# Kernel tuning notes

Hardware: AMD Instinct MI355X
Metric: run time of the kernel (lower is better)

Reference implementation:

```python
import jax, jax.numpy as jnp
import numpy as np

B, T, P, D, H, L, C = 32, 50000, 100, 512, 16, 6, 256
SCALES = [1, 2, 4]
NS = len(SCALES)
HS = H // NS          # heads per scale = 5
KD = D // H           # key_dim = 32
N = T // P            # num_patches = 500
FF = 4 * D
EPS = 1e-3            # keras LayerNormalization default epsilon


def layernorm(x, g, b):
    m = jnp.mean(x, axis=-1, keepdims=True)
    v = jnp.var(x, axis=-1, keepdims=True)
    return (x - m) * jax.lax.rsqrt(v + EPS) * g + b


def mha(x, Wq, bq, Wk, bk, Wv, bv, Wo, bo):
    # keras MultiHeadAttention: self-attention, scale 1/sqrt(key_dim), biases on
    q = jnp.einsum('bnd,dhk->bnhk', x, Wq) + bq
    k = jnp.einsum('bnd,dhk->bnhk', x, Wk) + bk
    v = jnp.einsum('bnd,dhk->bnhk', x, Wv) + bv
    scores = jnp.einsum('bnhk,bmhk->bhnm', q, k) / jnp.sqrt(jnp.asarray(KD, x.dtype))
    p = jax.nn.softmax(scores, axis=-1)
    o = jnp.einsum('bhnm,bmhk->bnhk', p, v)
    return jnp.einsum('bnhk,hkd->bnd', o, Wo) + bo


def forward(inputs, ln_in_g, ln_in_b, patch_W, patch_b, pos_emb,
            Wq, bq, Wk, bk, Wv, bv, Wo, bo, Wc, bc,
            ln1_g, ln1_b, W1, b1, W2, b2, ln2_g, ln2_b, head_W, head_b):
    x = inputs[..., None]                       # (B, T, 1)
    x = layernorm(x, ln_in_g, ln_in_b)          # degenerate size-1 LN (faithful)
    patches = x.reshape(B, N, P)                # (B, N, P)
    h = patches @ patch_W + patch_b + pos_emb   # (B, N, D)
    for l in range(L):
        outs = []
        for si, s in enumerate(SCALES):
            if s > 1:
                pooled = h.reshape(B, N // s, s, D).mean(axis=2)  # SAME avg_pool1d (N % s == 0)
            else:
                pooled = h
            a = mha(pooled, Wq[l, si], bq[l, si], Wk[l, si], bk[l, si],
                    Wv[l, si], bv[l, si], Wo[l, si], bo[l, si])
            if s > 1:
                a = jnp.repeat(a, s, axis=1)[:, :N]
            outs.append(a)
        comb = jnp.concatenate(outs, axis=-1) @ Wc[l] + bc[l]
        h = h + comb
        h = layernorm(h, ln1_g[l], ln1_b[l])
        f = jax.nn.gelu(h @ W1[l] + b1[l], approximate=False)
        f = f @ W2[l] + b2[l]
        h = h + f
        h = layernorm(h, ln2_g[l], ln2_b[l])
        # Dropout(0.1) identity at inference
    g = h.mean(axis=1)                          # GlobalAveragePooling1D
    return jax.nn.softmax(g @ head_W + head_b, axis=-1)  # key head


def setup_inputs() -> dict:
    key = jax.random.key(0)
    ks = jax.random.split(key, 20)
    r = lambda k, sh, s=0.02: (jax.random.normal(k, sh, jnp.float32) * s)
    f32 = jnp.float32
    return {
        'inputs': jax.random.normal(ks[0], (B, T), f32),
        'ln_in_g': jnp.ones((1,), f32),
        'ln_in_b': r(ks[1], (1,)),
        'patch_W': r(ks[2], (P, D)),
        'patch_b': r(ks[3], (D,)),
        'pos_emb': r(ks[4], (1, N, D)),
        'Wq': r(ks[5], (L, NS, D, HS, KD)), 'bq': jnp.zeros((L, NS, HS, KD), f32),
        'Wk': r(ks[6], (L, NS, D, HS, KD)), 'bk': jnp.zeros((L, NS, HS, KD), f32),
        'Wv': r(ks[7], (L, NS, D, HS, KD)), 'bv': jnp.zeros((L, NS, HS, KD), f32),
        'Wo': r(ks[8], (L, NS, HS, KD, D)), 'bo': jnp.zeros((L, NS, D), f32),
        'Wc': r(ks[9], (L, NS * D, D)), 'bc': jnp.zeros((L, D), f32),
        'ln1_g': jnp.ones((L, D), f32), 'ln1_b': jnp.zeros((L, D), f32),
        'W1': r(ks[10], (L, D, FF)), 'b1': jnp.zeros((L, FF), f32),
        'W2': r(ks[11], (L, FF, D)), 'b2': jnp.zeros((L, D), f32),
        'ln2_g': jnp.ones((L, D), f32), 'ln2_b': jnp.zeros((L, D), f32),
        'head_W': r(ks[12], (D, C)), 'head_b': jnp.zeros((C,), f32),
    }


def reference(inputs, ln_in_g, ln_in_b, patch_W, patch_b, pos_emb,
              Wq, bq, Wk, bk, Wv, bv, Wo, bo, Wc, bc,
              ln1_g, ln1_b, W1, b1, W2, b2, ln2_g, ln2_b, head_W, head_b):
    return forward(inputs, ln_in_g, ln_in_b, patch_W, patch_b, pos_emb,
                   Wq, bq, Wk, bk, Wv, bv, Wo, bo, Wc, bc,
                   ln1_g, ln1_b, W1, b1, W2, b2, ln2_g, ln2_b, head_W, head_b)
```

## Files before the change

### kernel.cpp

```cpp
#include <hip/hip_runtime.h>
#include <math.h>


#define DD 512
#define NN 500
#define HSC 5
#define KDD 32
#define QKVN 160
#define QKV3 480
#define FF 2048
#define NL 6
#define NC 256
#define NB 32
#define LNEPS 1e-3f
#define BM 128
#define BN 64
#define KCHB 64

#define AOFF1 256000
#define AOFF2 384000
#define RTOT 875
#define OSZ 140000
#define MLSZ 4384
#define QSP 420000

typedef __attribute__((ext_vector_type(8))) short bf16x8;
typedef __attribute__((ext_vector_type(4))) float f32x4;

__device__ __forceinline__ float gelu_exact(float x) {
    return 0.5f * x * (1.0f + erff(x * 0.70710678118654752f));
}

__device__ __forceinline__ unsigned int pkbf(float a, float b) {
    unsigned int r;
    asm("v_cvt_pk_bf16_f32 %0, %1, %2" : "=v"(r) : "v"(a), "v"(b));
    return r;
}


template<int POOL, int GATHER, int TAIL>
__device__ __forceinline__ void mstage(
        const float* __restrict__ A, int lda,
        const float* __restrict__ Bcol, int ldb,
        int M, int bm, int k0, int klim,
        int ar4, int akq, int bkq,
        float4 (&aR)[2][4], float4 (&bR)[4]) {
    #pragma unroll
    for (int p = 0; p < 2; ++p) {
        int row = min(bm + ar4 + p * 64, M - 1);
        const float* ap;
        if (!GATHER) {
            ap = A + (size_t)row * POOL * lda;
        } else {
            int si = k0 >> 9;
            ap = A + (si == 0 ? 0 : (si == 1 ? AOFF1 : AOFF2))
               + (size_t)(row >> si) * DD - (size_t)(k0 & ~(DD - 1));
        }
        #pragma unroll
        for (int i = 0; i < 4; ++i) {
            int kk = akq + i * 4;
            int kg = TAIL ? min(k0 + kk, klim - 4) : (k0 + kk);
            float4 v = *(const float4*)(ap + kg);
            #pragma unroll
            for (int t = 1; t < POOL; ++t) {
                float4 u = *(const float4*)(ap + kg + (size_t)t * lda);
                v.x += u.x; v.y += u.y; v.z += u.z; v.w += u.w;
            }
            if (POOL > 1) {
                const float ip = 1.0f / (float)POOL;
                v.x *= ip; v.y *= ip; v.z *= ip; v.w *= ip;
            }
            if (TAIL) {
                bool ok = (k0 + kk) < klim;
                v.x = ok ? v.x : 0.f; v.y = ok ? v.y : 0.f;
                v.z = ok ? v.z : 0.f; v.w = ok ? v.w : 0.f;
            }
            aR[p][i] = v;
        }
    }
    #pragma unroll
    for (int i = 0; i < 4; ++i) {
        int kr = TAIL ? min(k0 + bkq + i, klim - 1) : (k0 + bkq + i);
        bR[i] = *(const float4*)(Bcol + (size_t)kr * ldb);
    }
}

template<int POOL, int GATHER, int TAIL>
__device__ __forceinline__ void mfma_core(
        const float* __restrict__ A, int lda,
        const float* __restrict__ Bcol, int ldb,
        int M, int bm, int ks, int nch, int klim, f32x4 (&acc)[4][2]) {
    __shared__ __align__(16) unsigned short As[128 * 64];
    __shared__ __align__(16) unsigned short Bs[64 * 64];
    const int tid = threadIdx.x;
    const int ar4 = tid >> 2, akq = (tid & 3) * 16;
    const int bkq = (tid >> 4) * 4, bn4 = tid & 15;
    const int lane = tid & 63, wid = tid >> 6;
    const int wm = wid >> 1, wn = wid & 1;

    float4 aR[2][4], bR[4];
    mstage<POOL, GATHER, TAIL>(A, lda, Bcol, ldb, M, bm, ks, klim,
                               ar4, akq, bkq, aR, bR);

    for (int c = 0; c < nch; ++c) {
        __syncthreads();
        #pragma unroll
        for (int p = 0; p < 2; ++p) {
            int r = ar4 + p * 64;
            int swz = (r & 7) << 4;
            char* base = (char*)As + r * 128;
            #pragma unroll
            for (int i = 0; i < 4; ++i) {
                int cb = (akq + i * 4) * 2;
                *(uint2*)(base + (cb ^ swz)) = make_uint2(
                    pkbf(aR[p][i].x, aR[p][i].y), pkbf(aR[p][i].z, aR[p][i].w));
            }
        }
        {
            const float* b0 = (const float*)&bR[0];
            const float* b1 = (const float*)&bR[1];
            const float* b2 = (const float*)&bR[2];
            const float* b3 = (const float*)&bR[3];
            #pragma unroll
            for (int j = 0; j < 4; ++j) {
                int nrow = bn4 * 4 + j;
                char* base = (char*)Bs + nrow * 128;
                *(uint2*)(base + ((bkq * 2) ^ ((nrow & 7) << 4))) = make_uint2(
                    pkbf(b0[j], b1[j]), pkbf(b2[j], b3[j]));
            }
        }
        __syncthreads();
        if (c + 1 < nch)
            mstage<POOL, GATHER, TAIL>(A, lda, Bcol, ldb, M, bm,
                                       ks + (c + 1) * KCHB, klim,
                                       ar4, akq, bkq, aR, bR);
        #pragma unroll
        for (int half = 0; half < 2; ++half) {
            const int kb = (half * 32 + (lane >> 4) * 8) * 2;
            bf16x8 af[4], bf[2];
            #pragma unroll
            for (int m = 0; m < 4; ++m) {
                int r = wm * 64 + m * 16 + (lane & 15);
                af[m] = *(const bf16x8*)((const char*)As + r * 128 + (kb ^ ((r & 7) << 4)));
            }
            #pragma unroll
            for (int n = 0; n < 2; ++n) {
                int r = wn * 32 + n * 16 + (lane & 15);
                bf[n] = *(const bf16x8*)((const char*)Bs + r * 128 + (kb ^ ((r & 7) << 4)));
            }
            #pragma unroll
            for (int m = 0; m < 4; ++m)
                #pragma unroll
                for (int n = 0; n < 2; ++n)
                    acc[m][n] = __builtin_amdgcn_mfma_f32_16x16x32_bf16(
                        af[m], bf[n], acc[m][n], 0, 0, 0);
        }
    }
}

#define MACC_INIT(acc) { _Pragma("unroll") for (int m_ = 0; m_ < 4; ++m_) \
    _Pragma("unroll") for (int n_ = 0; n_ < 2; ++n_) \
    _Pragma("unroll") for (int j_ = 0; j_ < 4; ++j_) acc[m_][n_][j_] = 0.f; }

__global__ void colsum_kernel(const float* __restrict__ pw, float* __restrict__ csum) {
    int d = blockIdx.x * blockDim.x + threadIdx.x;
    if (d < DD) {
        float s = 0.f;
        for (int p = 0; p < 100; ++p) s += pw[p * DD + d];
        csum[d] = s;
    }
}

__global__ void init_h(const float* __restrict__ csum, const float* __restrict__ pb,
                       const float* __restrict__ pos, const float* __restrict__ lnb,
                       float* __restrict__ h) {
    int idx = blockIdx.x * 256 + threadIdx.x;
    if (idx >= NN * DD) return;
    int d = idx & (DD - 1);
    h[idx] = lnb[0] * csum[d] + pb[d] + pos[idx];
}

__global__ __launch_bounds__(256, 2) void qkv_part(
        const float* __restrict__ h,
        const float* __restrict__ Wq, const float* __restrict__ Wk,
        const float* __restrict__ Wv,
        float* __restrict__ part, int l) {
    int scale = blockIdx.z >> 2, ps = blockIdx.z & 3;
    int n = NN >> scale;
    int bm = blockIdx.y * BM;
    if (bm >= n) return;
    int bn = blockIdx.x * BN;
    size_t w = (size_t)(l * 3 + scale);
    int tid = threadIdx.x;
    int col = min(bn + (tid & 15) * 4, QKV3 - 4);
    int which = (col >= 320) ? 2 : ((col >= 160) ? 1 : 0);
    const float* Wsel = (which == 0) ? Wq : ((which == 1) ? Wk : Wv);
    const float* Bcol = Wsel + w * DD * QKVN + (col - which * QKVN);
    float* outb = part + (size_t)ps * QSP
                + (scale == 0 ? 0 : (scale == 1 ? 240000 : 360000));

    f32x4 acc[4][2];
    MACC_INIT(acc);
    if (scale == 0)
        mfma_core<1, 0, 0>(h, DD, Bcol, QKVN, n, bm, ps * 128, 2, DD, acc);
    else if (scale == 1)
        mfma_core<2, 0, 0>(h, DD, Bcol, QKVN, n, bm, ps * 128, 2, DD, acc);
    else
        mfma_core<4, 0, 0>(h, DD, Bcol, QKVN, n, bm, ps * 128, 2, DD, acc);

    int lane = tid & 63, wid = tid >> 6, wm = wid >> 1, wn = wid & 1;
    #pragma unroll
    for (int q = 0; q < 2; ++q) {
        int cb = bn + wn * 32 + q * 16;
        if (cb >= QKV3) continue;
        int c2 = cb + (lane & 15);
        #pragma unroll
        for (int m = 0; m < 4; ++m) {
            int r0 = bm + wm * 64 + m * 16 + ((lane >> 4) << 2);
            #pragma unroll
            for (int j = 0; j < 4; ++j) {
                int r = r0 + j;
                if (r < n) outb[(size_t)r * QKV3 + c2] = acc[m][q][j];
            }
        }
    }
}

__global__ void qkv_reduce(const float* __restrict__ part,
                           const float* __restrict__ bq,
                           const float* __restrict__ bk,
                           const float* __restrict__ bv,
                           float* __restrict__ qkvAll, int l) {
    int idx = blockIdx.x * 256 + threadIdx.x;
    if (idx >= 420000) return;
    int scale, base;
    if (idx < 240000) { scale = 0; base = 0; }
    else if (idx < 360000) { scale = 1; base = 240000; }
    else { scale = 2; base = 360000; }
    int rowrem = (idx - base) % QKV3;
    int which = rowrem / QKVN;
    int col = rowrem - which * QKVN;
    float v = part[idx] + part[QSP + idx]
            + part[2 * QSP + idx] + part[3 * QSP + idx];
    v += ((which == 0) ? bq : (which == 1 ? bk : bv))[(size_t)(l * 3 + scale) * QKVN + col];
    qkvAll[idx] = v;
}

__global__ __launch_bounds__(256, 2) void attn_split(
        const float* __restrict__ qkvAll, float* __restrict__ oPart,
        float* __restrict__ mPart, float* __restrict__ lPart) {
    int z = blockIdx.z;
    int scale, sp;
    if (z < 8)       { scale = 0; sp = z; }
    else if (z < 12) { scale = 1; sp = z - 8; }
    else             { scale = 2; sp = z - 12; }
    int n = NN >> scale;
    int qt = blockIdx.x;
    if (qt * 64 >= n) return;
    int hh = blockIdx.y;
    int ks = sp * 64;
    int ke = min(n, ks + 64);
    const float* qkv = qkvAll + (scale == 0 ? 0 : (scale == 1 ? 240000 : 360000));
    int rowb = (scale == 0 ? 0 : (scale == 1 ? 500 : 750));

    int tid = threadIdx.x;
    int kg = tid & 7, qq = tid >> 3;
    int q0 = qt * 64 + qq, q1 = q0 + 32;
    bool ok0 = q0 < n, ok1 = q1 < n;

    float qa[32], qb[32];
    {
        const float* p0 = qkv + (size_t)(ok0 ? q0 : 0) * QKV3 + hh * KDD;
        const float* p1 = qkv + (size_t)(ok1 ? q1 : 0) * QKV3 + hh * KDD;
        #pragma unroll
        for (int c4 = 0; c4 < 8; ++c4) {
            float4 v0 = *(const float4*)(p0 + c4 * 4);
            float4 v1 = *(const float4*)(p1 + c4 * 4);
            qa[c4 * 4] = v0.x; qa[c4 * 4 + 1] = v0.y; qa[c4 * 4 + 2] = v0.z; qa[c4 * 4 + 3] = v0.w;
            qb[c4 * 4] = v1.x; qb[c4 * 4 + 1] = v1.y; qb[c4 * 4 + 2] = v1.z; qb[c4 * 4 + 3] = v1.w;
        }
    }

    __shared__ float Ks[64][36];
    __shared__ float Vs[64][36];
    float o0[32], o1[32];
    #pragma unroll
    for (int c = 0; c < 32; ++c) { o0[c] = 0.f; o1[c] = 0.f; }
    float m0 = -1e30f, m1 = -1e30f, l0 = 0.f, l1 = 0.f;

    int srow = tid >> 2, scol = tid & 3;

    {
        int kc = ks;
        int krow = kc + srow;
        bool ok = krow < ke;
        const float* kp = qkv + (size_t)(ok ? krow : 0) * QKV3 + QKVN + hh * KDD;
        #pragma unroll
        for (int half = 0; half < 2; ++half) {
            int cc = (half * 4 + scol) * 4;
            float4 kv = ok ? *(const float4*)(kp + cc) : make_float4(0.f, 0.f, 0.f, 0.f);
            float4 vv = ok ? *(const float4*)(kp + QKVN + cc) : make_float4(0.f, 0.f, 0.f, 0.f);
            Ks[srow][cc] = kv.x; Ks[srow][cc + 1] = kv.y; Ks[srow][cc + 2] = kv.z; Ks[srow][cc + 3] = kv.w;
            Vs[srow][cc] = vv.x; Vs[srow][cc + 1] = vv.y; Vs[srow][cc + 2] = vv.z; Vs[srow][cc + 3] = vv.w;
        }
        __syncthreads();

        float p0[8], p1[8];
        float cm = -1e30f;
        #pragma unroll
        for (int jj = 0; jj < 8; ++jj) {
            int j = jj * 8 + kg;
            float s0 = 0.f, s1 = 0.f;
            #pragma unroll
            for (int c4 = 0; c4 < 8; ++c4) {
                float4 kv = *(const float4*)&Ks[j][c4 * 4];
                s0 += qa[c4 * 4] * kv.x + qa[c4 * 4 + 1] * kv.y
                    + qa[c4 * 4 + 2] * kv.z + qa[c4 * 4 + 3] * kv.w;
                s1 += qb[c4 * 4] * kv.x + qb[c4 * 4 + 1] * kv.y
                    + qb[c4 * 4 + 2] * kv.z + qb[c4 * 4 + 3] * kv.w;
            }
            s0 *= 0.17677669529663687f;
            s1 *= 0.17677669529663687f;
            if (kc + j >= ke) { s0 = -1e30f; s1 = -1e30f; }
            p0[jj] = s0; p1[jj] = s1;
            cm = fmaxf(cm, fmaxf(s0, s1));
        }
        cm = fmaxf(cm, __shfl_xor(cm, 1));
        cm = fmaxf(cm, __shfl_xor(cm, 2));
        cm = fmaxf(cm, __shfl_xor(cm, 4));

        m0 = cm; m1 = cm;
        #pragma unroll
        for (int jj = 0; jj < 8; ++jj) {
            p0[jj] = expf(p0[jj] - cm); l0 += p0[jj];
            p1[jj] = expf(p1[jj] - cm); l1 += p1[jj];
        }
        #pragma unroll
        for (int jj = 0; jj < 8; ++jj) {
            int j = jj * 8 + kg;
            float w0 = p0[jj], w1 = p1[jj];
            #pragma unroll
            for (int c4 = 0; c4 < 8; ++c4) {
                float4 vv = *(const float4*)&Vs[j][c4 * 4];
                o0[c4 * 4]     += w0 * vv.x; o0[c4 * 4 + 1] += w0 * vv.y;
                o0[c4 * 4 + 2] += w0 * vv.z; o0[c4 * 4 + 3] += w0 * vv.w;
                o1[c4 * 4]     += w1 * vv.x; o1[c4 * 4 + 1] += w1 * vv.y;
                o1[c4 * 4 + 2] += w1 * vv.z; o1[c4 * 4 + 3] += w1 * vv.w;
            }
        }
    }
    #pragma unroll
    for (int st = 1; st < 8; st <<= 1) {
        l0 += __shfl_xor(l0, st);
        l1 += __shfl_xor(l1, st);
        #pragma unroll
        for (int c = 0; c < 32; ++c) {
            o0[c] += __shfl_xor(o0[c], st);
            o1[c] += __shfl_xor(o1[c], st);
        }
    }
    if (kg == 0) {
        float* ob = oPart + (size_t)sp * OSZ;
        if (ok0) {
            int r = rowb + q0;
            float* op = ob + (size_t)r * QKVN + hh * KDD;
            #pragma unroll
            for (int c4 = 0; c4 < 8; ++c4) {
                float4 v; v.x = o0[c4*4]; v.y = o0[c4*4+1]; v.z = o0[c4*4+2]; v.w = o0[c4*4+3];
                *(float4*)(op + c4 * 4) = v;
            }
            mPart[sp * MLSZ + r * HSC + hh] = m0;
            lPart[sp * MLSZ + r * HSC + hh] = l0;
        }
        if (ok1) {
            int r = rowb + q1;
            float* op = ob + (size_t)r * QKVN + hh * KDD;
            #pragma unroll
            for (int c4 = 0; c4 < 8; ++c4) {
                float4 v; v.x = o1[c4*4]; v.y = o1[c4*4+1]; v.z = o1[c4*4+2]; v.w = o1[c4*4+3];
                *(float4*)(op + c4 * 4) = v;
            }
            mPart[sp * MLSZ + r * HSC + hh] = m1;
            lPart[sp * MLSZ + r * HSC + hh] = l1;
        }
    }
}

__global__ void attn_combine(const float* __restrict__ oPart,
                             const float* __restrict__ mPart,
                             const float* __restrict__ lPart,
                             float* __restrict__ oAll) {
    int idx = blockIdx.x * 256 + threadIdx.x;
    if (idx >= OSZ) return;
    int rh = idx >> 5;
    int r = rh / HSC, hh = rh - r * HSC;
    int scale = (r < 500) ? 0 : (r < 750 ? 1 : 2);
    int ns = 8 >> scale;
    float M = -1e30f;
    for (int s = 0; s < ns; ++s) M = fmaxf(M, mPart[s * MLSZ + r * HSC + hh]);
    float L = 0.f, val = 0.f;
    for (int s = 0; s < ns; ++s) {
        float wgt = expf(mPart[s * MLSZ + r * HSC + hh] - M);
        L += wgt * lPart[s * MLSZ + r * HSC + hh];
        val += wgt * oPart[(size_t)s * OSZ + idx];
    }
    oAll[idx] = val / L;
}

__global__ __launch_bounds__(256, 2) void wo_all(
        const float* __restrict__ oAll, const float* __restrict__ Wo,
        const float* __restrict__ bo, float* __restrict__ aAll, int l) {
    int z = blockIdx.z;
    int n = NN >> z;
    int bm = blockIdx.y * BM;
    if (bm >= n) return;
    int bn = blockIdx.x * BN;
    size_t w = (size_t)(l * 3 + z);
    const float* A = oAll + (z == 0 ? 0 : (z == 1 ? 80000 : 120000));
    float* C = aAll + (z == 0 ? 0 : (z == 1 ? AOFF1 : AOFF2));
    int tid = threadIdx.x;
    const float* Bcol = Wo + w * QKVN * DD + bn + (tid & 15) * 4;

    f32x4 acc[4][2];
    MACC_INIT(acc);
    mfma_core<1, 0, 32>(A, QKVN, Bcol, DD, n, bm, 0, 3, QKVN, acc);

    const float* bias = bo + w * DD;
    int lane = tid & 63, wid = tid >> 6, wm = wid >> 1, wn = wid & 1;
    #pragma unroll
    for (int q = 0; q < 2; ++q) {
        int c2 = bn + wn * 32 + q * 16 + (lane & 15);
        float bv_ = bias[c2];
        #pragma unroll
        for (int m = 0; m < 4; ++m) {
            int r0 = bm + wm * 64 + m * 16 + ((lane >> 4) << 2);
            #pragma unroll
            for (int j = 0; j < 4; ++j) {
                int r = r0 + j;
                if (r < n) C[(size_t)r * DD + c2] = acc[m][q][j] + bv_;
            }
        }
    }
}

__global__ __launch_bounds__(256, 2) void comb_part(
        const float* __restrict__ aAll, const float* __restrict__ Wc,
        float* __restrict__ part) {
    int zz = blockIdx.z;
    int bm = blockIdx.y * BM, bn = blockIdx.x * BN;
    int tid = threadIdx.x;
    const float* Bcol = Wc + bn + (tid & 15) * 4;
    f32x4 acc[4][2];
    MACC_INIT(acc);
    mfma_core<1, 1, 0>(aAll, DD, Bcol, DD, NN, bm, zz * 128, 2, 1536, acc);

    float* pz = part + (size_t)zz * NN * DD;
    int lane = tid & 63, wid = tid >> 6, wm = wid >> 1, wn = wid & 1;
    #pragma unroll
    for (int q = 0; q < 2; ++q) {
        int c2 = bn + wn * 32 + q * 16 + (lane & 15);
        #pragma unroll
        for (int m = 0; m < 4; ++m) {
            int r0 = bm + wm * 64 + m * 16 + ((lane >> 4) << 2);
            #pragma unroll
            for (int j = 0; j < 4; ++j) {
                int r = r0 + j;
                if (r < NN) pz[(size_t)r * DD + c2] = acc[m][q][j];
            }
        }
    }
}

__global__ __launch_bounds__(256, 2) void w1_part(
        const float* __restrict__ h, const float* __restrict__ W1,
        float* __restrict__ part) {
    int sp = blockIdx.z;
    int bm = blockIdx.y * BM, bn = blockIdx.x * BN;
    int tid = threadIdx.x;
    const float* Bcol = W1 + bn + (tid & 15) * 4;
    f32x4 acc[4][2];
    MACC_INIT(acc);
    mfma_core<1, 0, 0>(h, DD, Bcol, FF, NN, bm, sp * 128, 2, DD, acc);

    float* pz = part + (size_t)sp * NN * FF;
    int lane = tid & 63, wid = tid >> 6, wm = wid >> 1, wn = wid & 1;
    #pragma unroll
    for (int q = 0; q < 2; ++q) {
        int c2 = bn + wn * 32 + q * 16 + (lane & 15);
        #pragma unroll
        for (int m = 0; m < 4; ++m) {
            int r0 = bm + wm * 64 + m * 16 + ((lane >> 4) << 2);
            #pragma unroll
            for (int j = 0; j < 4; ++j) {
                int r = r0 + j;
                if (r < NN) pz[(size_t)r * FF + c2] = acc[m][q][j];
            }
        }
    }
}

__global__ void w1_reduce(const float* __restrict__ part,
                          const float* __restrict__ b1, float* __restrict__ f) {
    int idx = blockIdx.x * 256 + threadIdx.x;
    if (idx >= NN * FF) return;
    float v = part[idx] + part[NN * FF + idx]
            + part[2 * NN * FF + idx] + part[3 * NN * FF + idx];
    f[idx] = gelu_exact(v + b1[idx & (FF - 1)]);
}

__global__ __launch_bounds__(256, 2) void w2_part(
        const float* __restrict__ f, const float* __restrict__ W2,
        float* __restrict__ part) {
    int sp = blockIdx.z;
    int bm = blockIdx.y * BM, bn = blockIdx.x * BN;
    int tid = threadIdx.x;
    const float* Bcol = W2 + bn + (tid & 15) * 4;
    f32x4 acc[4][2];
    MACC_INIT(acc);
    mfma_core<1, 0, 0>(f, FF, Bcol, DD, NN, bm, sp * 128, 2, FF, acc);

    float* pz = part + (size_t)sp * NN * DD;
    int lane = tid & 63, wid = tid >> 6, wm = wid >> 1, wn = wid & 1;
    #pragma unroll
    for (int q = 0; q < 2; ++q) {
        int c2 = bn + wn * 32 + q * 16 + (lane & 15);
        #pragma unroll
        for (int m = 0; m < 4; ++m) {
            int r0 = bm + wm * 64 + m * 16 + ((lane >> 4) << 2);
            #pragma unroll
            for (int j = 0; j < 4; ++j) {
                int r = r0 + j;
                if (r < NN) pz[(size_t)r * DD + c2] = acc[m][q][j];
            }
        }
    }
}

__global__ void reduce_add_ln(const float* __restrict__ part, int S,
                              const float* __restrict__ bias,
                              float* __restrict__ h,
                              const float* __restrict__ gw,
                              const float* __restrict__ bw) {
    int row = blockIdx.x, t = threadIdx.x;
    size_t idx = (size_t)row * DD + t;
    float x = h[idx] + bias[t];
    for (int s = 0; s < S; ++s) x += part[(size_t)s * NN * DD + idx];
    int lane = t & 63, wv = t >> 6;
    __shared__ float s1[8], s2[8];
    __shared__ float mb[2];
    float sum = x, sq = x * x;
    for (int off = 32; off; off >>= 1) {
        sum += __shfl_down(sum, off);
        sq  += __shfl_down(sq,  off);
    }
    if (lane == 0) { s1[wv] = sum; s2[wv] = sq; }
    __syncthreads();
    if (t == 0) {
        float a = 0.f, b = 0.f;
        for (int i = 0; i < 8; ++i) { a += s1[i]; b += s2[i]; }
        float mean = a / (float)DD;
        float var = b / (float)DD - mean * mean;
        mb[0] = mean;
        mb[1] = rsqrtf(var + LNEPS);
    }
    __syncthreads();
    h[idx] = (x - mb[0]) * mb[1] * gw[t] + bw[t];
}

__global__ void col_mean_part(const float* __restrict__ h, float* __restrict__ partial) {
    int col = blockIdx.x * 256 + threadIdx.x;
    int r0 = blockIdx.y * 20;
    float s = 0.f;
    #pragma unroll
    for (int r = 0; r < 20; ++r) s += h[(size_t)(r0 + r) * DD + col];
    partial[(size_t)blockIdx.y * DD + col] = s;
}

__global__ void head_kernel(const float* __restrict__ partial,
                            const float* __restrict__ hw,
                            const float* __restrict__ hb, float* __restrict__ out) {
    __shared__ float gs[DD];
    __shared__ float r[4];
    __shared__ float bmx, bsum;
    int t = threadIdx.x;
    for (int d = t; d < DD; d += 256) {
        float s = 0.f;
        #pragma unroll
        for (int p = 0; p < 25; ++p) s += partial[(size_t)p * DD + d];
        gs[d] = s / (float)NN;
    }
    __syncthreads();
    float acc = hb[t];
    #pragma unroll 16
    for (int d = 0; d < DD; ++d) acc += gs[d] * hw[(size_t)d * NC + t];
    int lane = t & 63, wv = t >> 6;
    float mx = acc;
    for (int off = 32; off; off >>= 1) mx = fmaxf(mx, __shfl_down(mx, off));
    if (lane == 0) r[wv] = mx;
    __syncthreads();
    if (t == 0) bmx = fmaxf(fmaxf(r[0], r[1]), fmaxf(r[2], r[3]));
    __syncthreads();
    float e = expf(acc - bmx);
    float s = e;
    for (int off = 32; off; off >>= 1) s += __shfl_down(s, off);
    if (lane == 0) r[wv] = s;
    __syncthreads();
    if (t == 0) bsum = 1.f / (r[0] + r[1] + r[2] + r[3]);
    __syncthreads();
    float pv = e * bsum;
    for (int b = 0; b < NB; ++b) out[(size_t)b * NC + t] = pv;
}

extern "C" void kernel_launch(void* const* d_in, const int* in_sizes, int n_in,
                              void* d_out, int out_size, void* d_ws, size_t ws_size,
                              hipStream_t stream) {
    const float* ln_in_b = (const float*)d_in[2];
    const float* patch_W = (const float*)d_in[3];
    const float* patch_b = (const float*)d_in[4];
    const float* pos_emb = (const float*)d_in[5];
    const float* Wq = (const float*)d_in[6];
    const float* bq = (const float*)d_in[7];
    const float* Wk = (const float*)d_in[8];
    const float* bk = (const float*)d_in[9];
    const float* Wv = (const float*)d_in[10];
    const float* bv = (const float*)d_in[11];
    const float* Wo = (const float*)d_in[12];
    const float* bo = (const float*)d_in[13];
    const float* Wc = (const float*)d_in[14];
    const float* bc = (const float*)d_in[15];
    const float* ln1_g = (const float*)d_in[16];
    const float* ln1_b = (const float*)d_in[17];
    const float* W1 = (const float*)d_in[18];
    const float* b1 = (const float*)d_in[19];
    const float* W2 = (const float*)d_in[20];
    const float* b2 = (const float*)d_in[21];
    const float* ln2_g = (const float*)d_in[22];
    const float* ln2_b = (const float*)d_in[23];
    const float* head_W = (const float*)d_in[24];
    const float* head_b = (const float*)d_in[25];
    float* out = (float*)d_out;

    float* ws = (float*)d_ws;
    float* h      = ws;
    float* csum   = h + 256000;
    float* qkvAll = csum + 1024;
    float* oAll   = qkvAll + 420000;
    float* aAll   = oAll + 140000;
    float* f      = aAll + 448000;
    float* part   = f + 1024000;
    float* headp  = part + 4194304;
    float* qkvP   = part;
    float* oPart  = part + 1680000;
    float* mPart  = oPart + 1120000;
    float* lPart  = mPart + 8 * MLSZ;

    colsum_kernel<<<1, 512, 0, stream>>>(patch_W, csum);
    init_h<<<(NN * DD + 255) / 256, 256, 0, stream>>>(csum, patch_b, pos_emb, ln_in_b, h);

    for (int l = 0; l < NL; ++l) {
        qkv_part<<<dim3(8, 4, 12), 256, 0, stream>>>(h, Wq, Wk, Wv, qkvP, l);
        qkv_reduce<<<(420000 + 255) / 256, 256, 0, stream>>>(qkvP, bq, bk, bv, qkvAll, l);
        attn_split<<<dim3(8, HSC, 14), 256, 0, stream>>>(qkvAll, oPart, mPart, lPart);
        attn_combine<<<(OSZ + 255) / 256, 256, 0, stream>>>(oPart, mPart, lPart, oAll);
        wo_all<<<dim3(8, 4, 3), 256, 0, stream>>>(oAll, Wo, bo, aAll, l);
        comb_part<<<dim3(8, 4, 12), 256, 0, stream>>>(
            aAll, Wc + (size_t)l * 3 * DD * DD, part);
        reduce_add_ln<<<NN, DD, 0, stream>>>(part, 12, bc + (size_t)l * DD, h,
                                             ln1_g + (size_t)l * DD, ln1_b + (size_t)l * DD);
        w1_part<<<dim3(32, 4, 4), 256, 0, stream>>>(
            h, W1 + (size_t)l * DD * FF, part);
        w1_reduce<<<(NN * FF + 255) / 256, 256, 0, stream>>>(
            part, b1 + (size_t)l * FF, f);
        w2_part<<<dim3(8, 4, 16), 256, 0, stream>>>(f, W2 + (size_t)l * FF * DD, part);
        reduce_add_ln<<<NN, DD, 0, stream>>>(part, 16, b2 + (size_t)l * DD, h,
                                             ln2_g + (size_t)l * DD, ln2_b + (size_t)l * DD);
    }
    col_mean_part<<<dim3(2, 25), 256, 0, stream>>>(h, headp);
    head_kernel<<<1, 256, 0, stream>>>(headp, head_W, head_b, out);
}
```

Baseline: 783.6 us.

## Fold Wo into Wc weights so attention outputs feed the combine GEMM directly

```diff
diff --git a/kernel.cpp b/kernel.cpp
--- a/kernel.cpp
+++ b/kernel.cpp
@@ -17,12 +17,11 @@
 #define BN 64
 #define KCHB 64
 
-#define AOFF1 256000
-#define AOFF2 384000
 #define RTOT 875
 #define OSZ 140000
 #define MLSZ 4384
 #define QSP 420000
+#define W2CL 98304
 
 typedef __attribute__((ext_vector_type(8))) short bf16x8;
 typedef __attribute__((ext_vector_type(4))) float f32x4;
@@ -38,7 +37,7 @@
 }
 
 
-template<int POOL, int GATHER, int TAIL>
+template<int POOL, int TAIL>
 __device__ __forceinline__ void mstage(
         const float* __restrict__ A, int lda,
         const float* __restrict__ Bcol, int ldb,
@@ -48,14 +47,7 @@
     #pragma unroll
     for (int p = 0; p < 2; ++p) {
         int row = min(bm + ar4 + p * 64, M - 1);
-        const float* ap;
-        if (!GATHER) {
-            ap = A + (size_t)row * POOL * lda;
-        } else {
-            int si = k0 >> 9;
-            ap = A + (si == 0 ? 0 : (si == 1 ? AOFF1 : AOFF2))
-               + (size_t)(row >> si) * DD - (size_t)(k0 & ~(DD - 1));
-        }
+        const float* ap = A + (size_t)row * POOL * lda;
         #pragma unroll
         for (int i = 0; i < 4; ++i) {
             int kk = akq + i * 4;
@@ -85,7 +77,57 @@
     }
 }
 
-template<int POOL, int GATHER, int TAIL>
+#define CHUNK_LDS_WRITE() { \
+    _Pragma("unroll") \
+    for (int p = 0; p < 2; ++p) { \
+        int r = ar4 + p * 64; \
+        int swz = (r & 7) << 4; \
+        char* base = (char*)As + r * 128; \
+        _Pragma("unroll") \
+        for (int i = 0; i < 4; ++i) { \
+            int cb = (akq + i * 4) * 2; \
+            *(uint2*)(base + (cb ^ swz)) = make_uint2( \
+                pkbf(aR[p][i].x, aR[p][i].y), pkbf(aR[p][i].z, aR[p][i].w)); \
+        } \
+    } \
+    { \
+        const float* b0 = (const float*)&bR[0]; \
+        const float* b1 = (const float*)&bR[1]; \
+        const float* b2 = (const float*)&bR[2]; \
+        const float* b3 = (const float*)&bR[3]; \
+        _Pragma("unroll") \
+        for (int j = 0; j < 4; ++j) { \
+            int nrow = bn4 * 4 + j; \
+            char* base = (char*)Bs + nrow * 128; \
+            *(uint2*)(base + ((bkq * 2) ^ ((nrow & 7) << 4))) = make_uint2( \
+                pkbf(b0[j], b1[j]), pkbf(b2[j], b3[j])); \
+        } \
+    } }
+
+#define CHUNK_MFMA() { \
+    _Pragma("unroll") \
+    for (int half = 0; half < 2; ++half) { \
+        const int kb = (half * 32 + (lane >> 4) * 8) * 2; \
+        bf16x8 af[4], bf[2]; \
+        _Pragma("unroll") \
+        for (int m = 0; m < 4; ++m) { \
+            int r = wm * 64 + m * 16 + (lane & 15); \
+            af[m] = *(const bf16x8*)((const char*)As + r * 128 + (kb ^ ((r & 7) << 4))); \
+        } \
+        _Pragma("unroll") \
+        for (int n = 0; n < 2; ++n) { \
+            int r = wn * 32 + n * 16 + (lane & 15); \
+            bf[n] = *(const bf16x8*)((const char*)Bs + r * 128 + (kb ^ ((r & 7) << 4))); \
+        } \
+        _Pragma("unroll") \
+        for (int m = 0; m < 4; ++m) \
+            _Pragma("unroll") \
+            for (int n = 0; n < 2; ++n) \
+                acc[m][n] = __builtin_amdgcn_mfma_f32_16x16x32_bf16( \
+                    af[m], bf[n], acc[m][n], 0, 0, 0); \
+    } }
+
+template<int POOL, int TAIL>
 __device__ __forceinline__ void mfma_core(
         const float* __restrict__ A, int lda,
         const float* __restrict__ Bcol, int ldb,
@@ -99,62 +141,18 @@
     const int wm = wid >> 1, wn = wid & 1;
 
     float4 aR[2][4], bR[4];
-    mstage<POOL, GATHER, TAIL>(A, lda, Bcol, ldb, M, bm, ks, klim,
-                               ar4, akq, bkq, aR, bR);
+    mstage<POOL, TAIL>(A, lda, Bcol, ldb, M, bm, ks, klim,
+                       ar4, akq, bkq, aR, bR);
 
     for (int c = 0; c < nch; ++c) {
         __syncthreads();
-        #pragma unroll
-        for (int p = 0; p < 2; ++p) {
-            int r = ar4 + p * 64;
-            int swz = (r & 7) << 4;
-            char* base = (char*)As + r * 128;
-            #pragma unroll
-            for (int i = 0; i < 4; ++i) {
-                int cb = (akq + i * 4) * 2;
-                *(uint2*)(base + (cb ^ swz)) = make_uint2(
-                    pkbf(aR[p][i].x, aR[p][i].y), pkbf(aR[p][i].z, aR[p][i].w));
-            }
-        }
-        {
-            const float* b0 = (const float*)&bR[0];
-            const float* b1 = (const float*)&bR[1];
-            const float* b2 = (const float*)&bR[2];
-            const float* b3 = (const float*)&bR[3];
-            #pragma unroll
-            for (int j = 0; j < 4; ++j) {
-                int nrow = bn4 * 4 + j;
-                char* base = (char*)Bs + nrow * 128;
-                *(uint2*)(base + ((bkq * 2) ^ ((nrow & 7) << 4))) = make_uint2(
-                    pkbf(b0[j], b1[j]), pkbf(b2[j], b3[j]));
-            }
-        }
+        CHUNK_LDS_WRITE();
         __syncthreads();
         if (c + 1 < nch)
-            mstage<POOL, GATHER, TAIL>(A, lda, Bcol, ldb, M, bm,
-                                       ks + (c + 1) * KCHB, klim,
-                                       ar4, akq, bkq, aR, bR);
-        #pragma unroll
-        for (int half = 0; half < 2; ++half) {
-            const int kb = (half * 32 + (lane >> 4) * 8) * 2;
-            bf16x8 af[4], bf[2];
-            #pragma unroll
-            for (int m = 0; m < 4; ++m) {
-                int r = wm * 64 + m * 16 + (lane & 15);
-                af[m] = *(const bf16x8*)((const char*)As + r * 128 + (kb ^ ((r & 7) << 4)));
-            }
-            #pragma unroll
-            for (int n = 0; n < 2; ++n) {
-                int r = wn * 32 + n * 16 + (lane & 15);
-                bf[n] = *(const bf16x8*)((const char*)Bs + r * 128 + (kb ^ ((r & 7) << 4)));
-            }
-            #pragma unroll
-            for (int m = 0; m < 4; ++m)
-                #pragma unroll
-                for (int n = 0; n < 2; ++n)
-                    acc[m][n] = __builtin_amdgcn_mfma_f32_16x16x32_bf16(
-                        af[m], bf[n], acc[m][n], 0, 0, 0);
-        }
+            mstage<POOL, TAIL>(A, lda, Bcol, ldb, M, bm,
+                               ks + (c + 1) * KCHB, klim,
+                               ar4, akq, bkq, aR, bR);
+        CHUNK_MFMA();
     }
 }
 
@@ -178,6 +176,51 @@
     if (idx >= NN * DD) return;
     int d = idx & (DD - 1);
     h[idx] = lnb[0] * csum[d] + pb[d] + pos[idx];
+}
+
+__global__ __launch_bounds__(256, 2) void w2c_pre(
+        const float* __restrict__ Wo, const float* __restrict__ Wc,
+        float* __restrict__ w2c) {
+    int z = blockIdx.z;
+    int l = z / 3, s = z - l * 3;
+    int bm = blockIdx.y * BM, bn = blockIdx.x * BN;
+    int tid = threadIdx.x;
+    const float* A = Wo + (size_t)z * QKVN * DD;
+    const float* Bcol = Wc + (size_t)l * 1536 * DD + (size_t)s * DD * DD
+                      + bn + (tid & 15) * 4;
+    f32x4 acc[4][2];
+    MACC_INIT(acc);
+    mfma_core<1, 0>(A, DD, Bcol, DD, QKVN, bm, 0, 8, DD, acc);
+
+    float* C = w2c + (size_t)z * W2CL;
+    int lane = tid & 63, wid = tid >> 6, wm = wid >> 1, wn = wid & 1;
+    #pragma unroll
+    for (int q = 0; q < 2; ++q) {
+        int c2 = bn + wn * 32 + q * 16 + (lane & 15);
+        #pragma unroll
+        for (int m = 0; m < 4; ++m) {
+            int r0 = bm + wm * 64 + m * 16 + ((lane >> 4) << 2);
+            #pragma unroll
+            for (int j = 0; j < 4; ++j) {
+                int r = r0 + j;
+                if (r < QKVN) C[(size_t)r * DD + c2] = acc[m][q][j];
+                else if (r < 192) C[(size_t)r * DD + c2] = 0.f;
+            }
+        }
+    }
+}
+
+__global__ void bconst_pre(const float* __restrict__ bo, const float* __restrict__ Wc,
+                           const float* __restrict__ bc, float* __restrict__ bconst) {
+    int l = blockIdx.x, d = threadIdx.x;
+    float acc = bc[(size_t)l * DD + d];
+    for (int s = 0; s < 3; ++s) {
+        const float* bp = bo + (size_t)(l * 3 + s) * DD;
+        const float* wp = Wc + (size_t)l * 1536 * DD + (size_t)s * DD * DD + d;
+        for (int j = 0; j < DD; ++j)
+            acc += bp[j] * wp[(size_t)j * DD];
+    }
+    bconst[(size_t)l * DD + d] = acc;
 }
 
 __global__ __launch_bounds__(256, 2) void qkv_part(
@@ -202,11 +245,11 @@
     f32x4 acc[4][2];
     MACC_INIT(acc);
     if (scale == 0)
-        mfma_core<1, 0, 0>(h, DD, Bcol, QKVN, n, bm, ps * 128, 2, DD, acc);
+        mfma_core<1, 0>(h, DD, Bcol, QKVN, n, bm, ps * 128, 2, DD, acc);
     else if (scale == 1)
-        mfma_core<2, 0, 0>(h, DD, Bcol, QKVN, n, bm, ps * 128, 2, DD, acc);
+        mfma_core<2, 0>(h, DD, Bcol, QKVN, n, bm, ps * 128, 2, DD, acc);
     else
-        mfma_core<4, 0, 0>(h, DD, Bcol, QKVN, n, bm, ps * 128, 2, DD, acc);
+        mfma_core<4, 0>(h, DD, Bcol, QKVN, n, bm, ps * 128, 2, DD, acc);
 
     int lane = tid & 63, wid = tid >> 6, wm = wid >> 1, wn = wid & 1;
     #pragma unroll
@@ -407,55 +450,50 @@
     oAll[idx] = val / L;
 }
 
-__global__ __launch_bounds__(256, 2) void wo_all(
-        const float* __restrict__ oAll, const float* __restrict__ Wo,
-        const float* __restrict__ bo, float* __restrict__ aAll, int l) {
-    int z = blockIdx.z;
-    int n = NN >> z;
-    int bm = blockIdx.y * BM;
-    if (bm >= n) return;
-    int bn = blockIdx.x * BN;
-    size_t w = (size_t)(l * 3 + z);
-    const float* A = oAll + (z == 0 ? 0 : (z == 1 ? 80000 : 120000));
-    float* C = aAll + (z == 0 ? 0 : (z == 1 ? AOFF1 : AOFF2));
+__global__ __launch_bounds__(256, 2) void comb_gather(
+        const float* __restrict__ oAll, const float* __restrict__ w2c,
+        float* __restrict__ part, int l) {
+    int sp = blockIdx.z;
+    int si = (sp >= 6) ? 2 : (sp >= 3 ? 1 : 0);
+    int kseg = (sp - si * 3) << 6;
+    int bm = blockIdx.y * BM, bn = blockIdx.x * BN;
     int tid = threadIdx.x;
-    const float* Bcol = Wo + w * QKVN * DD + bn + (tid & 15) * 4;
+    const int soff = (si == 0) ? 0 : (si == 1 ? 80000 : 120000);
+    const float* Bcol = w2c + (size_t)(l * 3 + si) * W2CL
+                      + (size_t)kseg * DD + bn + (tid & 15) * 4;
+
+    __shared__ __align__(16) unsigned short As[128 * 64];
+    __shared__ __align__(16) unsigned short Bs[64 * 64];
+    const int ar4 = tid >> 2, akq = (tid & 3) * 16;
+    const int bkq = (tid >> 4) * 4, bn4 = tid & 15;
+    const int lane = tid & 63, wid = tid >> 6;
+    const int wm = wid >> 1, wn = wid & 1;
 
     f32x4 acc[4][2];
     MACC_INIT(acc);
-    mfma_core<1, 0, 32>(A, QKVN, Bcol, DD, n, bm, 0, 3, QKVN, acc);
-
-    const float* bias = bo + w * DD;
-    int lane = tid & 63, wid = tid >> 6, wm = wid >> 1, wn = wid & 1;
-    #pragma unroll
-    for (int q = 0; q < 2; ++q) {
-        int c2 = bn + wn * 32 + q * 16 + (lane & 15);
-        float bv_ = bias[c2];
-        #pragma unroll
-        for (int m = 0; m < 4; ++m) {
-            int r0 = bm + wm * 64 + m * 16 + ((lane >> 4) << 2);
-            #pragma unroll
-            for (int j = 0; j < 4; ++j) {
-                int r = r0 + j;
-                if (r < n) C[(size_t)r * DD + c2] = acc[m][q][j] + bv_;
-            }
-        }
-    }
-}
-
-__global__ __launch_bounds__(256, 2) void comb_part(
-        const float* __restrict__ aAll, const float* __restrict__ Wc,
-        float* __restrict__ part) {
-    int zz = blockIdx.z;
-    int bm = blockIdx.y * BM, bn = blockIdx.x * BN;
-    int tid = threadIdx.x;
-    const float* Bcol = Wc + bn + (tid & 15) * 4;
-    f32x4 acc[4][2];
-    MACC_INIT(acc);
-    mfma_core<1, 1, 0>(aAll, DD, Bcol, DD, NN, bm, zz * 128, 2, 1536, acc);
-
-    float* pz = part + (size_t)zz * NN * DD;
-    int lane = tid & 63, wid = tid >> 6, wm = wid >> 1, wn = wid & 1;
+    float4 aR[2][4], bR[4];
+
+    #pragma unroll
+    for (int p = 0; p < 2; ++p) {
+        int row = min(bm + ar4 + p * 64, NN - 1);
+        const float* ap = oAll + soff + (size_t)(row >> si) * QKVN;
+        #pragma unroll
+        for (int i = 0; i < 4; ++i) {
+            int kk = kseg + akq + i * 4;
+            int kg2 = min(kk, QKVN - 4);
+            aR[p][i] = *(const float4*)(ap + kg2);
+        }
+    }
+    #pragma unroll
+    for (int i = 0; i < 4; ++i)
+        bR[i] = *(const float4*)(Bcol + (size_t)(bkq + i) * DD);
+
+    __syncthreads();
+    CHUNK_LDS_WRITE();
+    __syncthreads();
+    CHUNK_MFMA();
+
+    float* pz = part + (size_t)sp * NN * DD;
     #pragma unroll
     for (int q = 0; q < 2; ++q) {
         int c2 = bn + wn * 32 + q * 16 + (lane & 15);
@@ -480,7 +518,7 @@
     const float* Bcol = W1 + bn + (tid & 15) * 4;
     f32x4 acc[4][2];
     MACC_INIT(acc);
-    mfma_core<1, 0, 0>(h, DD, Bcol, FF, NN, bm, sp * 128, 2, DD, acc);
+    mfma_core<1, 0>(h, DD, Bcol, FF, NN, bm, sp * 128, 2, DD, acc);
 
     float* pz = part + (size_t)sp * NN * FF;
     int lane = tid & 63, wid = tid >> 6, wm = wid >> 1, wn = wid & 1;
@@ -517,7 +555,7 @@
     const float* Bcol = W2 + bn + (tid & 15) * 4;
     f32x4 acc[4][2];
     MACC_INIT(acc);
-    mfma_core<1, 0, 0>(f, FF, Bcol, DD, NN, bm, sp * 128, 2, FF, acc);
+    mfma_core<1, 0>(f, FF, Bcol, DD, NN, bm, sp * 128, 2, FF, acc);
 
     float* pz = part + (size_t)sp * NN * DD;
     int lane = tid & 63, wid = tid >> 6, wm = wid >> 1, wn = wid & 1;
@@ -645,10 +683,11 @@
     float* csum   = h + 256000;
     float* qkvAll = csum + 1024;
     float* oAll   = qkvAll + 420000;
-    float* aAll   = oAll + 140000;
-    float* f      = aAll + 448000;
+    float* f      = oAll + 140000;
     float* part   = f + 1024000;
     float* headp  = part + 4194304;
+    float* w2c    = headp + 12800;
+    float* bconst = w2c + 1769472;
     float* qkvP   = part;
     float* oPart  = part + 1680000;
     float* mPart  = oPart + 1120000;
@@ -656,16 +695,16 @@
 
     colsum_kernel<<<1, 512, 0, stream>>>(patch_W, csum);
     init_h<<<(NN * DD + 255) / 256, 256, 0, stream>>>(csum, patch_b, pos_emb, ln_in_b, h);
+    w2c_pre<<<dim3(8, 2, 18), 256, 0, stream>>>(Wo, Wc, w2c);
+    bconst_pre<<<NL, DD, 0, stream>>>(bo, Wc, bc, bconst);
 
     for (int l = 0; l < NL; ++l) {
         qkv_part<<<dim3(8, 4, 12), 256, 0, stream>>>(h, Wq, Wk, Wv, qkvP, l);
         qkv_reduce<<<(420000 + 255) / 256, 256, 0, stream>>>(qkvP, bq, bk, bv, qkvAll, l);
         attn_split<<<dim3(8, HSC, 14), 256, 0, stream>>>(qkvAll, oPart, mPart, lPart);
         attn_combine<<<(OSZ + 255) / 256, 256, 0, stream>>>(oPart, mPart, lPart, oAll);
-        wo_all<<<dim3(8, 4, 3), 256, 0, stream>>>(oAll, Wo, bo, aAll, l);
-        comb_part<<<dim3(8, 4, 12), 256, 0, stream>>>(
-            aAll, Wc + (size_t)l * 3 * DD * DD, part);
-        reduce_add_ln<<<NN, DD, 0, stream>>>(part, 12, bc + (size_t)l * DD, h,
+        comb_gather<<<dim3(8, 4, 9), 256, 0, stream>>>(oAll, w2c, part, l);
+        reduce_add_ln<<<NN, DD, 0, stream>>>(part, 9, bconst + (size_t)l * DD, h,
                                              ln1_g + (size_t)l * DD, ln1_b + (size_t)l * DD);
         w1_part<<<dim3(32, 4, 4), 256, 0, stream>>>(
             h, W1 + (size_t)l * DD * FF, part);
```

New measurement: 793.0 us. No clear change (+1.2%).
